# Optimization experiments

Measured on AMD Instinct MI355X. Metric: run time of the kernel, lower is better.

The kernel has to match this reference:

```python
import jax, jax.numpy as jnp
import numpy as np

B_SZ, IN_DIM, N_NEURONS, N_LAYERS, N_OUTS = 65536, 4, 512, 8, 4


def setup_inputs() -> dict:
    key = jax.random.key(0)
    ks = jax.random.split(key, 5)
    glorot = lambda k, shape: jax.random.normal(k, shape, jnp.float32) * np.sqrt(2.0 / (shape[-2] + shape[-1]))
    inputs = jax.random.normal(ks[0], (B_SZ, IN_DIM), jnp.float32)
    # GaussianRFF projection matrix (fixed random Gaussian)
    B_rff = jax.random.normal(ks[1], (IN_DIM, N_NEURONS // 2), jnp.float32)
    Ws = glorot(ks[2], (N_LAYERS, N_NEURONS, N_NEURONS))
    bs = jnp.zeros((N_LAYERS, N_NEURONS), jnp.float32)
    alphas = jnp.zeros((N_LAYERS + 1,), jnp.float32)  # LAAF slopes, init 0
    Wf = glorot(ks[3], (N_NEURONS, N_OUTS))           # final mixer, no bias
    scale = jnp.ones((N_OUTS,), jnp.float32)          # Scaler, no bias
    return {"inputs": inputs, "B_rff": B_rff, "Ws": Ws, "bs": bs,
            "alphas": alphas, "Wf": Wf, "scale": scale}


def _mlp(x, B_rff, Ws, bs, alphas, Wf, scale):
    # Gaussian random Fourier feature embedding -> [B, n_neurons]
    z = x @ B_rff
    u = jnp.concatenate([jnp.sin(z), jnp.cos(z)], axis=-1)
    L = Ws.shape[0]
    def step(u, p):
        W, b, a = p
        # LAAF sine layer: sin(w0 * (1 + alpha) * (uW + b)), w0 = 1.0
        return jnp.sin((1.0 + a) * (u @ W + b)), None
    u, _ = jax.lax.scan(step, u, (Ws, bs, alphas[:L]))
    return (u @ Wf) * scale  # [B, 4] = (A1, A2, A3, phi)


def reference(inputs, B_rff, Ws, bs, alphas, Wf, scale):
    f = lambda x: _mlp(x, B_rff, Ws, bs, alphas, Wf, scale)
    def jvp_col(col):
        tang = jnp.zeros_like(inputs).at[:, col].set(1.0)
        return jax.jvp(f, (inputs,), (tang,))
    # input columns: 0=t, 1=z, 2=x, 3=y
    P, dPdz = jvp_col(1)
    _, dPdx = jvp_col(2)
    _, dPdy = jvp_col(3)
    A1_y, A1_z = dPdy[:, 0:1], dPdz[:, 0:1]
    A2_x, A2_z = dPdx[:, 1:2], dPdz[:, 1:2]
    A3_x, A3_y = dPdx[:, 2:3], dPdy[:, 2:3]
    phi_x, phi_y, phi_z = dPdx[:, 3:4], dPdy[:, 3:4], dPdz[:, 3:4]
    u = (A3_y - A2_z) + phi_x
    v = (A1_z - A3_x) + phi_y
    w = (A2_x - A1_y) + phi_z
    return jnp.concatenate([u, v, w], axis=1)
```

## Files before the change

kernel.cpp:

```cpp
#include <hip/hip_runtime.h>
#include <stdint.h>


#define B_SZ   65536
#define NN     512
#define NL     8
#define SPB    16
#define MROWS  64
#define MT     4
#define NTW    4
#define NKB    16
#define NG     (NL*NKB)
#define LDS_A  (MROWS*1024)
#define LDS_TOTAL (LDS_A + 1024)

typedef _Float16 f16x8 __attribute__((ext_vector_type(8)));
typedef float    f32x4 __attribute__((ext_vector_type(4)));

__device__ __forceinline__ uint16_t f2h_bits(float f) {
  union { _Float16 h; uint16_t u; } v; v.h = (_Float16)f; return v.u;
}
__device__ __forceinline__ float h2f(uint16_t b) {
  union { uint16_t u; _Float16 h; } v; v.u = b; return (float)v.h;
}

__global__ __launch_bounds__(512) void prep_weights(const float* __restrict__ Ws,
                                                    uint16_t* __restrict__ img) {
  const int g  = blockIdx.x;
  const int l  = g >> 4, kb = g & 15;
  const float* src = Ws + ((size_t)l << 18);
  char* dst = (char*)img + ((size_t)g << 15);
  #pragma unroll
  for (int it = 0; it < 4; ++it) {
    const int fidx = threadIdx.x + it*512;
    const int ln  = fidx & 63, sub = fidx >> 6;
    const int n     = (sub >> 2)*64 + (sub & 3)*16 + (ln & 15);
    const int kbase = kb*32 + (ln >> 4)*8;
    uint16_t h[8];
    #pragma unroll
    for (int e = 0; e < 8; ++e)
      h[e] = f2h_bits(src[(size_t)(kbase + e)*512 + n]);
    uint4 pk;
    pk.x = (uint32_t)h[0] | ((uint32_t)h[1] << 16);
    pk.y = (uint32_t)h[2] | ((uint32_t)h[3] << 16);
    pk.z = (uint32_t)h[4] | ((uint32_t)h[5] << 16);
    pk.w = (uint32_t)h[6] | ((uint32_t)h[7] << 16);
    *(uint4*)(dst + (size_t)fidx*16) = pk;
  }
}

__global__ __launch_bounds__(512, 4) void pinn_fused(
    const float* __restrict__ inputs, const float* __restrict__ Brff,
    const float* __restrict__ bs, const float* __restrict__ alphas,
    const float* __restrict__ Wf, const float* __restrict__ scl,
    const uint16_t* __restrict__ wimg, float* __restrict__ out)
{
  extern __shared__ char smem[];

  const int tid  = threadIdx.x;
  const int lane = tid & 63;
  const int wv   = tid >> 6;
  const int i16  = lane & 15;
  const int q    = lane >> 4;
  const int sbase = blockIdx.x * SPB;

  {
    const int k = tid, col = k & 255;
    const bool iscos = (k >= 256);
    const float b0 = Brff[col];
    const float b1 = Brff[256 + col];
    const float b2 = Brff[512 + col];
    const float b3 = Brff[768 + col];
    const int koff = 2*k;
    for (int s = 0; s < SPB; ++s) {
      const float4 x = *(const float4*)(inputs + ((size_t)(sbase + s) << 2));
      const float z = x.x*b0 + x.y*b1 + x.z*b2 + x.w*b3;
      const float szn = __sinf(z), czn = __cosf(z);
      const float u0 = iscos ? czn : szn;
      const float dz = iscos ? -szn : czn;
      const int m0 = 4*s;
      *(uint16_t*)(smem + (size_t)(m0+0)*1024 + (koff ^ (((m0+0) & 7)*16))) = f2h_bits(u0);
      *(uint16_t*)(smem + (size_t)(m0+1)*1024 + (koff ^ (((m0+1) & 7)*16))) = f2h_bits(dz*b1);
      *(uint16_t*)(smem + (size_t)(m0+2)*1024 + (koff ^ (((m0+2) & 7)*16))) = f2h_bits(dz*b2);
      *(uint16_t*)(smem + (size_t)(m0+3)*1024 + (koff ^ (((m0+3) & 7)*16))) = f2h_bits(dz*b3);
    }
  }
  __syncthreads();

  const char* wbase = (const char*)wimg + ((size_t)wv << 12) + (size_t)lane*16;

  f16x8 bA[NTW], bB[NTW];
  #pragma unroll
  for (int Nt = 0; Nt < NTW; ++Nt)
    bA[Nt] = *(const f16x8*)(wbase + (size_t)Nt*1024);

  f32x4 acc[MT][NTW];

  for (int l = 0; l < NL; ++l) {
    const f32x4 zz = {0.f, 0.f, 0.f, 0.f};
    #pragma unroll
    for (int a = 0; a < MT; ++a)
      #pragma unroll
      for (int b = 0; b < NTW; ++b) acc[a][b] = zz;

    #pragma unroll 1
    for (int t = 0; t < NKB/2; ++t) {
      const int g = l*NKB + 2*t;
      {
        const char* p = wbase + ((size_t)(g + 1) << 15);
        #pragma unroll
        for (int Nt = 0; Nt < NTW; ++Nt) bB[Nt] = *(const f16x8*)(p + (size_t)Nt*1024);
      }
      {
        const int kb = 2*t;
        const int roff = (kb*64 + q*16) ^ ((i16 & 7)*16);
        #pragma unroll
        for (int Mt = 0; Mt < MT; ++Mt) {
          const f16x8 af = *(const f16x8*)(smem + (size_t)(Mt*16 + i16)*1024 + roff);
          #pragma unroll
          for (int Nt = 0; Nt < NTW; ++Nt)
            acc[Mt][Nt] = __builtin_amdgcn_mfma_f32_16x16x32_f16(af, bA[Nt], acc[Mt][Nt], 0, 0, 0);
        }
      }
      if (g + 2 < NG) {
        const char* p = wbase + ((size_t)(g + 2) << 15);
        #pragma unroll
        for (int Nt = 0; Nt < NTW; ++Nt) bA[Nt] = *(const f16x8*)(p + (size_t)Nt*1024);
      }
      {
        const int kb = 2*t + 1;
        const int roff = (kb*64 + q*16) ^ ((i16 & 7)*16);
        #pragma unroll
        for (int Mt = 0; Mt < MT; ++Mt) {
          const f16x8 af = *(const f16x8*)(smem + (size_t)(Mt*16 + i16)*1024 + roff);
          #pragma unroll
          for (int Nt = 0; Nt < NTW; ++Nt)
            acc[Mt][Nt] = __builtin_amdgcn_mfma_f32_16x16x32_f16(af, bB[Nt], acc[Mt][Nt], 0, 0, 0);
        }
      }
    }
    __syncthreads();

    const float opa = 1.0f + alphas[l];
    #pragma unroll
    for (int Nt = 0; Nt < NTW; ++Nt) {
      const int nc = wv*64 + Nt*16 + i16;
      const float bias = bs[l*NN + nc];
      #pragma unroll
      for (int Mt = 0; Mt < MT; ++Mt) {
        f32x4 c = acc[Mt][Nt];
        float h  = opa * (c[0] + bias);
        float un = __sinf(h);
        float fc = opa * __cosf(h);
        float vv[4] = { un, fc*c[1], fc*c[2], fc*c[3] };
        const int mb = Mt*16 + q*4;
        #pragma unroll
        for (int r = 0; r < 4; ++r) {
          const int m = mb + r;
          *(uint16_t*)(smem + (size_t)m*1024 + ((2*nc) ^ ((m & 7)*16))) = f2h_bits(vv[r]);
        }
      }
    }
    __syncthreads();
  }

  float* dp = (float*)(smem + LDS_A);
  const float4 sc4 = *(const float4*)scl;
  for (int rr = 0; rr < MROWS/8; ++rr) {
    const int m = wv*(MROWS/8) + rr;
    float p0 = 0.f, p1 = 0.f, p2 = 0.f, p3 = 0.f;
    #pragma unroll
    for (int j = 0; j < 8; ++j) {
      const int k = lane + j*64;
      float a = h2f(*(const uint16_t*)(smem + (size_t)m*1024 + ((2*k) ^ ((m & 7)*16))));
      float4 wf = ((const float4*)Wf)[k];
      p0 += a*wf.x; p1 += a*wf.y; p2 += a*wf.z; p3 += a*wf.w;
    }
    #pragma unroll
    for (int d = 1; d < 64; d <<= 1) {
      p0 += __shfl_xor(p0, d, 64);
      p1 += __shfl_xor(p1, d, 64);
      p2 += __shfl_xor(p2, d, 64);
      p3 += __shfl_xor(p3, d, 64);
    }
    if (lane == 0) {
      float4* o = (float4*)(dp + m*4);
      *o = make_float4(p0*sc4.x, p1*sc4.y, p2*sc4.z, p3*sc4.w);
    }
  }
  __syncthreads();

  if (tid < SPB*3) {
    const int sl = tid / 3, c = tid - sl*3;
    const float* d1 = dp + (sl*4 + 1)*4;
    const float* d2 = dp + (sl*4 + 2)*4;
    const float* d3 = dp + (sl*4 + 3)*4;
    float val;
    if (c == 0)      val = d3[2] - d1[1] + d2[3];
    else if (c == 1) val = d1[0] - d2[2] + d3[3];
    else             val = d2[1] - d3[0] + d1[3];
    out[(size_t)(sbase + sl)*3 + c] = val;
  }
}

extern "C" void kernel_launch(void* const* d_in, const int* in_sizes, int n_in,
                              void* d_out, int out_size, void* d_ws, size_t ws_size,
                              hipStream_t stream) {
  const float* inputs = (const float*)d_in[0];
  const float* Brff   = (const float*)d_in[1];
  const float* Ws     = (const float*)d_in[2];
  const float* bsp    = (const float*)d_in[3];
  const float* alph   = (const float*)d_in[4];
  const float* Wfp    = (const float*)d_in[5];
  const float* sclp   = (const float*)d_in[6];
  uint16_t* wimg = (uint16_t*)d_ws;

  prep_weights<<<NG, 512, 0, stream>>>(Ws, wimg);
  const int nblocks = B_SZ / SPB;
  pinn_fused<<<nblocks, 512, LDS_TOTAL, stream>>>(inputs, Brff, bsp, alph, Wfp, sclp,
                                                  wimg, (float*)d_out);
}
```

Baseline: 1.415 ms.

## Switch MLP GEMM to 32x32x16 MFMA tiles with double-buffered LDS A fragments

Replaces the 16x16x32 MFMA tiling (4x4 accumulators per wave) with 32x32x16 MFMA (2x2 accumulators), and reorganizes the prepacked weight image into 16-wide K slices to match. A-fragments from LDS are now double-buffered in registers, and the next layer's first fragments are prefetched after the barrier. s_setprio is wrapped around MFMA groups. The goal is fewer LDS reads per FLOP and better overlap, though it adds more serial K steps with smaller per-step weight loads.

Result: faster. 1.343 ms (-5.1%).

```diff
diff --git a/kernel.cpp b/kernel.cpp
--- a/kernel.cpp
+++ b/kernel.cpp
@@ -7,15 +7,13 @@
 #define NL     8
 #define SPB    16
 #define MROWS  64
-#define MT     4
-#define NTW    4
-#define NKB    16
-#define NG     (NL*NKB)
+#define NKS    32
+#define NG2    (NL*NKS)
 #define LDS_A  (MROWS*1024)
 #define LDS_TOTAL (LDS_A + 1024)
 
-typedef _Float16 f16x8 __attribute__((ext_vector_type(8)));
-typedef float    f32x4 __attribute__((ext_vector_type(4)));
+typedef _Float16 f16x8  __attribute__((ext_vector_type(8)));
+typedef float    f32x16 __attribute__((ext_vector_type(16)));
 
 __device__ __forceinline__ uint16_t f2h_bits(float f) {
   union { _Float16 h; uint16_t u; } v; v.h = (_Float16)f; return v.u;
@@ -26,16 +24,16 @@
 
 __global__ __launch_bounds__(512) void prep_weights(const float* __restrict__ Ws,
                                                     uint16_t* __restrict__ img) {
-  const int g  = blockIdx.x;
-  const int l  = g >> 4, kb = g & 15;
+  const int g2 = blockIdx.x;
+  const int l  = g2 >> 5, ks = g2 & 31;
   const float* src = Ws + ((size_t)l << 18);
-  char* dst = (char*)img + ((size_t)g << 15);
+  char* dst = (char*)img + ((size_t)g2 << 14);
   #pragma unroll
-  for (int it = 0; it < 4; ++it) {
+  for (int it = 0; it < 2; ++it) {
     const int fidx = threadIdx.x + it*512;
     const int ln  = fidx & 63, sub = fidx >> 6;
-    const int n     = (sub >> 2)*64 + (sub & 3)*16 + (ln & 15);
-    const int kbase = kb*32 + (ln >> 4)*8;
+    const int n     = (sub >> 1)*64 + (sub & 1)*32 + (ln & 31);
+    const int kbase = ks*16 + (ln >> 5)*8;
     uint16_t h[8];
     #pragma unroll
     for (int e = 0; e < 8; ++e)
@@ -60,9 +58,16 @@
   const int tid  = threadIdx.x;
   const int lane = tid & 63;
   const int wv   = tid >> 6;
-  const int i16  = lane & 15;
-  const int q    = lane >> 4;
+  const int l31  = lane & 31;
+  const int kh   = lane >> 5;
   const int sbase = blockIdx.x * SPB;
+
+  const char* wb = (const char*)wimg + ((size_t)(wv*2) << 10) + (size_t)lane*16;
+
+  f16x8 bfA0 = *(const f16x8*)(wb);
+  f16x8 bfA1 = *(const f16x8*)(wb + 1024);
+  f16x8 bfB0 = *(const f16x8*)(wb + 16384);
+  f16x8 bfB1 = *(const f16x8*)(wb + 16384 + 1024);
 
   {
     const int k = tid, col = k & 255;
@@ -87,55 +92,60 @@
   }
   __syncthreads();
 
-  const char* wbase = (const char*)wimg + ((size_t)wv << 12) + (size_t)lane*16;
-
-  f16x8 bA[NTW], bB[NTW];
-  #pragma unroll
-  for (int Nt = 0; Nt < NTW; ++Nt)
-    bA[Nt] = *(const f16x8*)(wbase + (size_t)Nt*1024);
-
-  f32x4 acc[MT][NTW];
+  const int rx   = (l31 & 7) * 16;
+  const int hoff = kh * 16;
+  char* arow0 = smem + (size_t)l31 * 1024;
+  char* arow1 = arow0 + 32*1024;
+
+  f16x8 afA0 = *(const f16x8*)(arow0 + (hoff ^ rx));
+  f16x8 afA1 = *(const f16x8*)(arow1 + (hoff ^ rx));
+  f16x8 afB0, afB1;
+
+  const f32x16 zz = {0,0,0,0,0,0,0,0,0,0,0,0,0,0,0,0};
 
   for (int l = 0; l < NL; ++l) {
-    const f32x4 zz = {0.f, 0.f, 0.f, 0.f};
-    #pragma unroll
-    for (int a = 0; a < MT; ++a)
-      #pragma unroll
-      for (int b = 0; b < NTW; ++b) acc[a][b] = zz;
+    f32x16 a00 = zz, a01 = zz, a10 = zz, a11 = zz;
+    const int g2b = l*NKS;
 
     #pragma unroll 1
-    for (int t = 0; t < NKB/2; ++t) {
-      const int g = l*NKB + 2*t;
+    for (int t = 0; t < NKS/2; ++t) {
+      const int ks = 2*t;
       {
-        const char* p = wbase + ((size_t)(g + 1) << 15);
-        #pragma unroll
-        for (int Nt = 0; Nt < NTW; ++Nt) bB[Nt] = *(const f16x8*)(p + (size_t)Nt*1024);
-      }
+        const int co = ((ks + 1)*32 + hoff) ^ rx;
+        afB0 = *(const f16x8*)(arow0 + co);
+        afB1 = *(const f16x8*)(arow1 + co);
+      }
+      __builtin_amdgcn_s_setprio(1);
+      a00 = __builtin_amdgcn_mfma_f32_32x32x16_f16(afA0, bfA0, a00, 0, 0, 0);
+      a01 = __builtin_amdgcn_mfma_f32_32x32x16_f16(afA0, bfA1, a01, 0, 0, 0);
+      a10 = __builtin_amdgcn_mfma_f32_32x32x16_f16(afA1, bfA0, a10, 0, 0, 0);
+      a11 = __builtin_amdgcn_mfma_f32_32x32x16_f16(afA1, bfA1, a11, 0, 0, 0);
+      __builtin_amdgcn_s_setprio(0);
       {
-        const int kb = 2*t;
-        const int roff = (kb*64 + q*16) ^ ((i16 & 7)*16);
-        #pragma unroll
-        for (int Mt = 0; Mt < MT; ++Mt) {
-          const f16x8 af = *(const f16x8*)(smem + (size_t)(Mt*16 + i16)*1024 + roff);
-          #pragma unroll
-          for (int Nt = 0; Nt < NTW; ++Nt)
-            acc[Mt][Nt] = __builtin_amdgcn_mfma_f32_16x16x32_f16(af, bA[Nt], acc[Mt][Nt], 0, 0, 0);
+        const int gt = g2b + ks + 2;
+        if (gt < NG2) {
+          const char* p = wb + ((size_t)gt << 14);
+          bfA0 = *(const f16x8*)(p);
+          bfA1 = *(const f16x8*)(p + 1024);
         }
       }
-      if (g + 2 < NG) {
-        const char* p = wbase + ((size_t)(g + 2) << 15);
-        #pragma unroll
-        for (int Nt = 0; Nt < NTW; ++Nt) bA[Nt] = *(const f16x8*)(p + (size_t)Nt*1024);
-      }
+      if (t + 1 < NKS/2) {
+        const int co = ((ks + 2)*32 + hoff) ^ rx;
+        afA0 = *(const f16x8*)(arow0 + co);
+        afA1 = *(const f16x8*)(arow1 + co);
+      }
+      __builtin_amdgcn_s_setprio(1);
+      a00 = __builtin_amdgcn_mfma_f32_32x32x16_f16(afB0, bfB0, a00, 0, 0, 0);
+      a01 = __builtin_amdgcn_mfma_f32_32x32x16_f16(afB0, bfB1, a01, 0, 0, 0);
+      a10 = __builtin_amdgcn_mfma_f32_32x32x16_f16(afB1, bfB0, a10, 0, 0, 0);
+      a11 = __builtin_amdgcn_mfma_f32_32x32x16_f16(afB1, bfB1, a11, 0, 0, 0);
+      __builtin_amdgcn_s_setprio(0);
       {
-        const int kb = 2*t + 1;
-        const int roff = (kb*64 + q*16) ^ ((i16 & 7)*16);
-        #pragma unroll
-        for (int Mt = 0; Mt < MT; ++Mt) {
-          const f16x8 af = *(const f16x8*)(smem + (size_t)(Mt*16 + i16)*1024 + roff);
-          #pragma unroll
-          for (int Nt = 0; Nt < NTW; ++Nt)
-            acc[Mt][Nt] = __builtin_amdgcn_mfma_f32_16x16x32_f16(af, bB[Nt], acc[Mt][Nt], 0, 0, 0);
+        const int gt = g2b + ks + 3;
+        if (gt < NG2) {
+          const char* p = wb + ((size_t)gt << 14);
+          bfB0 = *(const f16x8*)(p);
+          bfB1 = *(const f16x8*)(p + 1024);
         }
       }
     }
@@ -143,25 +153,34 @@
 
     const float opa = 1.0f + alphas[l];
     #pragma unroll
-    for (int Nt = 0; Nt < NTW; ++Nt) {
-      const int nc = wv*64 + Nt*16 + i16;
+    for (int Nt = 0; Nt < 2; ++Nt) {
+      const int nc = wv*64 + Nt*32 + l31;
       const float bias = bs[l*NN + nc];
       #pragma unroll
-      for (int Mt = 0; Mt < MT; ++Mt) {
-        f32x4 c = acc[Mt][Nt];
-        float h  = opa * (c[0] + bias);
-        float un = __sinf(h);
-        float fc = opa * __cosf(h);
-        float vv[4] = { un, fc*c[1], fc*c[2], fc*c[3] };
-        const int mb = Mt*16 + q*4;
+      for (int Mt = 0; Mt < 2; ++Mt) {
+        const f32x16 c = (Mt == 0) ? (Nt == 0 ? a00 : a01)
+                                   : (Nt == 0 ? a10 : a11);
         #pragma unroll
-        for (int r = 0; r < 4; ++r) {
-          const int m = mb + r;
-          *(uint16_t*)(smem + (size_t)m*1024 + ((2*nc) ^ ((m & 7)*16))) = f2h_bits(vv[r]);
+        for (int j = 0; j < 4; ++j) {
+          const float hh = opa * (c[4*j] + bias);
+          const float un = __sinf(hh);
+          const float fc = opa * __cosf(hh);
+          const float vv[4] = { un, fc*c[4*j+1], fc*c[4*j+2], fc*c[4*j+3] };
+          const int m0 = Mt*32 + 8*j + 4*kh;
+          #pragma unroll
+          for (int s = 0; s < 4; ++s) {
+            const int m = m0 + s;
+            *(uint16_t*)(smem + (size_t)m*1024 + ((2*nc) ^ ((m & 7)*16))) = f2h_bits(vv[s]);
+          }
         }
       }
     }
     __syncthreads();
+
+    if (l + 1 < NL) {
+      afA0 = *(const f16x8*)(arow0 + (hoff ^ rx));
+      afA1 = *(const f16x8*)(arow1 + (hoff ^ rx));
+    }
   }
 
   float* dp = (float*)(smem + LDS_A);
@@ -215,7 +234,7 @@
   const float* sclp   = (const float*)d_in[6];
   uint16_t* wimg = (uint16_t*)d_ws;
 
-  prep_weights<<<NG, 512, 0, stream>>>(Ws, wimg);
+  prep_weights<<<NG2, 512, 0, stream>>>(Ws, wimg);
   const int nblocks = B_SZ / SPB;
   pinn_fused<<<nblocks, 512, LDS_TOTAL, stream>>>(inputs, Brff, bsp, alph, Wfp, sclp,
                                                   wimg, (float*)d_out);
```
